# Performance work log

Hardware: AMD Instinct MI355X
Metric: run time of the kernel (lower is better)

## Reference

```python
import jax, jax.numpy as jnp
import numpy as np

N = 50000      # nodes
E = 600000     # edges
G = 512        # graphs in batch
F_IN = 128     # input node features
H = 128        # hidden size (both layers)
PH = 128       # pool/classifier hidden size


def setup_inputs() -> dict:
    key = jax.random.key(0)
    ks = jax.random.split(key, 12)
    def lin(k, fi, fo):
        return (jax.random.normal(k, (fi, fo), jnp.float32) / np.sqrt(fi)).astype(jnp.float32)
    return {
        "x": jax.random.normal(ks[0], (N, F_IN), jnp.float32),
        "edge_index": jax.random.randint(ks[1], (2, E), 0, N),
        "batch": jnp.sort(jax.random.randint(ks[2], (N,), 0, G)),
        "W1": lin(ks[3], F_IN, H), "b1": jnp.zeros((H,), jnp.float32),
        "ln1_g": jnp.ones((H,), jnp.float32), "ln1_b": jnp.zeros((H,), jnp.float32),
        "W2": lin(ks[4], H, H), "b2": jnp.zeros((H,), jnp.float32),
        "ln2_g": jnp.ones((H,), jnp.float32), "ln2_b": jnp.zeros((H,), jnp.float32),
        "gate_w1": lin(ks[5], H, PH), "gate_b1": jnp.zeros((PH,), jnp.float32),
        "gate_w2": lin(ks[6], PH, 1), "gate_b2": jnp.zeros((1,), jnp.float32),
        "cls_w1": lin(ks[7], H, PH), "cls_b1": jnp.zeros((PH,), jnp.float32),
        "cls_w2": lin(ks[8], PH, 2), "cls_b2": jnp.zeros((2,), jnp.float32),
    }


def _layer_norm(h, g, b):
    m = h.mean(-1, keepdims=True)
    v = ((h - m) ** 2).mean(-1, keepdims=True)
    return (h - m) * jax.lax.rsqrt(v + 1e-5) * g + b


def _gcn(x, src, dst, norm, W, b):
    # GCNConv: x' = D^{-1/2} (A+I) D^{-1/2} (x W) + b
    h = x @ W
    out = jax.ops.segment_sum(h[src] * norm[:, None], dst, num_segments=N)
    return out + b


def reference(x, edge_index, batch, W1, b1, ln1_g, ln1_b, W2, b2, ln2_g, ln2_b,
              gate_w1, gate_b1, gate_w2, gate_b2, cls_w1, cls_b1, cls_w2, cls_b2):
    loops = jnp.arange(N, dtype=edge_index.dtype)
    src = jnp.concatenate([edge_index[0], loops])
    dst = jnp.concatenate([edge_index[1], loops])
    deg = jax.ops.segment_sum(jnp.ones_like(src, dtype=x.dtype), dst, num_segments=N)
    dinv = jnp.where(deg > 0, jax.lax.rsqrt(jnp.maximum(deg, 1e-12)), 0.0)
    norm = dinv[src] * dinv[dst]  # [(E+N)]

    h = jax.nn.relu(_layer_norm(_gcn(x, src, dst, norm, W1, b1), ln1_g, ln1_b))
    h = jax.nn.relu(_layer_norm(_gcn(h, src, dst, norm, W2, b2), ln2_g, ln2_b))

    # GlobalAttention pooling: gate MLP -> scatter softmax over graphs -> weighted sum
    gate = (jax.nn.relu(h @ gate_w1 + gate_b1) @ gate_w2 + gate_b2)[:, 0]  # [N]
    gmax = jax.ops.segment_max(gate, batch, num_segments=G)
    a = jnp.exp(gate - gmax[batch])
    denom = jax.ops.segment_sum(a, batch, num_segments=G)
    alpha = a / denom[batch]
    pooled = jax.ops.segment_sum(alpha[:, None] * h, batch, num_segments=G)  # [G, H]

    logits = jax.nn.relu(pooled @ cls_w1 + cls_b1) @ cls_w2 + cls_b2  # [G, 2]
    return logits
```

## Files before the change

kernel.cpp:

```cpp
#include <hip/hip_runtime.h>
#include <hip/hip_bf16.h>

typedef short s8v __attribute__((ext_vector_type(8)));
typedef float f4v __attribute__((ext_vector_type(4)));

__device__ __forceinline__ unsigned short f2bf(float f) {
  unsigned int u = __builtin_bit_cast(unsigned int, f);
  unsigned int r = u + 0x7fffu + ((u >> 16) & 1u);
  return (unsigned short)(r >> 16);
}
__device__ __forceinline__ float bf2f(unsigned short s) {
  return __builtin_bit_cast(float, ((unsigned int)s) << 16);
}
__device__ __forceinline__ float bflo(unsigned int v) {
  return __builtin_bit_cast(float, (unsigned int)(v << 16));
}
__device__ __forceinline__ float bfhi(unsigned int v) {
  return __builtin_bit_cast(float, (unsigned int)(v & 0xffff0000u));
}
__device__ __forceinline__ unsigned int packbf(float a, float b) {
  return (unsigned int)f2bf(a) | ((unsigned int)f2bf(b) << 16);
}

__device__ __forceinline__ int lower_bound_i(const int* a, int n, int key) {
  int lo = 0, hi = n;
  while (lo < hi) { int mid = (lo + hi) >> 1; if (a[mid] < key) lo = mid + 1; else hi = mid; }
  return lo;
}

__global__ __launch_bounds__(256) void pack_zero(
    const float* __restrict__ Wa, const float* __restrict__ Wb, const float* __restrict__ Wc,
    unsigned short* __restrict__ P, unsigned int* __restrict__ deg, int n) {
  int bid = blockIdx.x;
  if (bid >= 384) {
    int i = (bid - 384) * 256 + threadIdx.x;
    if (i < n) deg[i] = 0u;
    return;
  }
  int gidx = bid * 256 + threadIdx.x;
  int which = gidx >> 15;
  int idx = gidx & 32767;
  const float* W = (which == 0) ? Wa : (which == 1) ? Wb : Wc;
  int j = idx & 15;
  int lane = (idx >> 4) & 63;
  int t = (idx >> 10) & 7;
  int c = (idx >> 13) & 3;
  int k = c * 32 + (lane >> 4) * 8 + (j & 7);
  int nn = t * 16 + (lane & 15);
  float f = W[k * 128 + nn];
  unsigned short hi = f2bf(f);
  unsigned short outv = (j < 8) ? hi : f2bf(f - bf2f(hi));
  P[gidx] = outv;
}

__global__ void accum_deg(const int* __restrict__ dst, unsigned int* __restrict__ deg, int E) {
  int e = blockIdx.x * blockDim.x + threadIdx.x;
  if (e < E) atomicAdd(&deg[dst[e]], 1u);
}

__global__ __launch_bounds__(256) void scanA(const unsigned int* __restrict__ deg,
                                             int* __restrict__ offs, int* __restrict__ partial,
                                             float* __restrict__ dinv, int n) {
  __shared__ int sh[256];
  int t = threadIdx.x;
  int i = blockIdx.x * 256 + t;
  int v = (i < n) ? (int)deg[i] : 0;
  if (i < n) dinv[i] = rsqrtf((float)(deg[i] + 1u));
  sh[t] = v;
  __syncthreads();
  for (int o = 1; o < 256; o <<= 1) {
    int add = (t >= o) ? sh[t - o] : 0;
    __syncthreads();
    sh[t] += add;
    __syncthreads();
  }
  if (i < n) offs[i] = sh[t] - v;
  if (t == 255) partial[blockIdx.x] = sh[255];
}

__global__ __launch_bounds__(256) void scanC(int* __restrict__ offs, const int* __restrict__ partial,
                                             int* __restrict__ cursor, int n, int E) {
  __shared__ int red[256];
  int bid = blockIdx.x;
  int t = threadIdx.x;
  int s = 0;
  for (int j = t; j < bid; j += 256) s += partial[j];
  red[t] = s;
  __syncthreads();
#pragma unroll
  for (int o = 128; o > 0; o >>= 1) {
    if (t < o) red[t] += red[t + o];
    __syncthreads();
  }
  int pre = red[0];
  int i = bid * 256 + t;
  if (i < n) {
    int o = offs[i] + pre;
    offs[i] = o;
    cursor[i] = o;
  }
  if (i == 0) offs[n] = E;
}

__global__ __launch_bounds__(256) void gemm1_scatter(
    const float* __restrict__ in, const unsigned short* __restrict__ P,
    unsigned short* __restrict__ out, int n,
    const int* __restrict__ src, const int* __restrict__ dst,
    int* __restrict__ cursor, int2* __restrict__ col2,
    const float* __restrict__ dinv, int E, int gemmBlocks) {
  if ((int)blockIdx.x >= gemmBlocks) {
    int e = ((int)blockIdx.x - gemmBlocks) * 256 + threadIdx.x;
    if (e < E) {
      int d = dst[e];
      int s = src[e];
      int slot = atomicAdd(&cursor[d], 1);
      col2[slot] = make_int2(s, __builtin_bit_cast(int, dinv[s]));
    }
    return;
  }
  int tid = threadIdx.x;
  int wave = tid >> 6, lane = tid & 63;
  int quad = lane >> 4, col = lane & 15;
  int base = blockIdx.x * 64 + wave * 16;
  int m = base + col;

  f4v acc[8];
#pragma unroll
  for (int t = 0; t < 8; ++t) acc[t] = (f4v){0.f, 0.f, 0.f, 0.f};

  for (int c = 0; c < 4; ++c) {
    s8v ah, al;
    float v[8];
    if (m < n) {
      const float4* xp = reinterpret_cast<const float4*>(in + (size_t)m * 128 + c * 32 + quad * 8);
      float4 v0 = xp[0], v1 = xp[1];
      v[0] = v0.x; v[1] = v0.y; v[2] = v0.z; v[3] = v0.w;
      v[4] = v1.x; v[5] = v1.y; v[6] = v1.z; v[7] = v1.w;
    } else {
#pragma unroll
      for (int j = 0; j < 8; ++j) v[j] = 0.f;
    }
#pragma unroll
    for (int j = 0; j < 8; ++j) {
      unsigned short h = f2bf(v[j]);
      ah[j] = (short)h;
      al[j] = (short)f2bf(v[j] - bf2f(h));
    }
#pragma unroll
    for (int t = 0; t < 8; ++t) {
      const s8v* bp = reinterpret_cast<const s8v*>(&P[((c * 8 + t) * 64 + lane) * 16]);
      s8v bh = bp[0], bl = bp[1];
      acc[t] = __builtin_amdgcn_mfma_f32_16x16x32_bf16(ah, bh, acc[t], 0, 0, 0);
      acc[t] = __builtin_amdgcn_mfma_f32_16x16x32_bf16(ah, bl, acc[t], 0, 0, 0);
      acc[t] = __builtin_amdgcn_mfma_f32_16x16x32_bf16(al, bh, acc[t], 0, 0, 0);
    }
  }
#pragma unroll
  for (int t = 0; t < 8; ++t)
#pragma unroll
    for (int r = 0; r < 4; ++r) {
      int mm = base + quad * 4 + r;
      if (mm < n) out[(size_t)mm * 128 + t * 16 + col] = f2bf(acc[t][r]);
    }
}

__global__ __launch_bounds__(256) void gemm_b16in(
    const unsigned short* __restrict__ in, const unsigned short* __restrict__ P,
    unsigned short* __restrict__ out, int n) {
  int tid = threadIdx.x;
  int wave = tid >> 6, lane = tid & 63;
  int quad = lane >> 4, col = lane & 15;
  int base = blockIdx.x * 64 + wave * 16;
  int m = base + col;

  f4v acc[8];
#pragma unroll
  for (int t = 0; t < 8; ++t) acc[t] = (f4v){0.f, 0.f, 0.f, 0.f};

  for (int c = 0; c < 4; ++c) {
    s8v ah;
    if (m < n)
      ah = *reinterpret_cast<const s8v*>(in + (size_t)m * 128 + c * 32 + quad * 8);
    else
      ah = (s8v){0, 0, 0, 0, 0, 0, 0, 0};
#pragma unroll
    for (int t = 0; t < 8; ++t) {
      const s8v* bp = reinterpret_cast<const s8v*>(&P[((c * 8 + t) * 64 + lane) * 16]);
      s8v bh = bp[0], bl = bp[1];
      acc[t] = __builtin_amdgcn_mfma_f32_16x16x32_bf16(ah, bh, acc[t], 0, 0, 0);
      acc[t] = __builtin_amdgcn_mfma_f32_16x16x32_bf16(ah, bl, acc[t], 0, 0, 0);
    }
  }
#pragma unroll
  for (int t = 0; t < 8; ++t)
#pragma unroll
    for (int r = 0; r < 4; ++r) {
      int mm = base + quad * 4 + r;
      if (mm < n) out[(size_t)mm * 128 + t * 16 + col] = f2bf(acc[t][r]);
    }
}

__global__ __launch_bounds__(256) void gemm_gate(
    const unsigned short* __restrict__ in, const unsigned short* __restrict__ P,
    const float* __restrict__ gb1, const float* __restrict__ gw2,
    const float* __restrict__ gb2, float* __restrict__ gate, int n) {
  int tid = threadIdx.x;
  int wave = tid >> 6, lane = tid & 63;
  int quad = lane >> 4, col = lane & 15;
  int base = blockIdx.x * 64 + wave * 16;
  int m = base + col;

  f4v acc[8];
#pragma unroll
  for (int t = 0; t < 8; ++t) acc[t] = (f4v){0.f, 0.f, 0.f, 0.f};

  for (int c = 0; c < 4; ++c) {
    s8v ah;
    if (m < n)
      ah = *reinterpret_cast<const s8v*>(in + (size_t)m * 128 + c * 32 + quad * 8);
    else
      ah = (s8v){0, 0, 0, 0, 0, 0, 0, 0};
#pragma unroll
    for (int t = 0; t < 8; ++t) {
      const s8v* bp = reinterpret_cast<const s8v*>(&P[((c * 8 + t) * 64 + lane) * 16]);
      s8v bh = bp[0], bl = bp[1];
      acc[t] = __builtin_amdgcn_mfma_f32_16x16x32_bf16(ah, bh, acc[t], 0, 0, 0);
      acc[t] = __builtin_amdgcn_mfma_f32_16x16x32_bf16(ah, bl, acc[t], 0, 0, 0);
    }
  }
  float bv[8], g2[8];
#pragma unroll
  for (int t = 0; t < 8; ++t) {
    bv[t] = gb1[t * 16 + col];
    g2[t] = gw2[t * 16 + col];
  }
  float gb2v = gb2[0];
#pragma unroll
  for (int r = 0; r < 4; ++r) {
    float p = 0.f;
#pragma unroll
    for (int t = 0; t < 8; ++t)
      p += fmaxf(acc[t][r] + bv[t], 0.f) * g2[t];
#pragma unroll
    for (int o = 1; o < 16; o <<= 1) p += __shfl_xor(p, o);
    int mm = base + quad * 4 + r;
    if (col == 0 && mm < n) gate[mm] = p + gb2v;
  }
}

__global__ __launch_bounds__(256) void gather_ln(
    const int* __restrict__ offs, const int2* __restrict__ col2,
    const float* __restrict__ dinv, const unsigned short* __restrict__ h,
    const float* __restrict__ bias, const float* __restrict__ gam,
    const float* __restrict__ bet, unsigned short* __restrict__ out, int n) {
  int wid = (int)((blockIdx.x * 256u + threadIdx.x) >> 6);
  int lane = threadIdx.x & 63;
  int grp = lane >> 4;
  int sub = lane & 15;
  int i = wid * 4 + grp;
  if (i >= n) return;
  const uint4* hu = reinterpret_cast<const uint4*>(h);
  float di = dinv[i];
  float sl = di * di;
  uint4 hv = hu[(size_t)i * 16 + sub];
  float4 b0v = reinterpret_cast<const float4*>(bias)[sub * 2];
  float4 b1v = reinterpret_cast<const float4*>(bias)[sub * 2 + 1];
  float v[8];
  v[0] = bflo(hv.x) * sl + b0v.x; v[1] = bfhi(hv.x) * sl + b0v.y;
  v[2] = bflo(hv.y) * sl + b0v.z; v[3] = bfhi(hv.y) * sl + b0v.w;
  v[4] = bflo(hv.z) * sl + b1v.x; v[5] = bfhi(hv.z) * sl + b1v.y;
  v[6] = bflo(hv.w) * sl + b1v.z; v[7] = bfhi(hv.w) * sl + b1v.w;
  int b0 = offs[i], b1 = offs[i + 1];
  int e = b0;
  for (; e + 4 <= b1; e += 4) {
    int2 c0 = col2[e], c1 = col2[e + 1], c2 = col2[e + 2], c3 = col2[e + 3];
    uint4 h0 = hu[(size_t)c0.x * 16 + sub];
    uint4 h1 = hu[(size_t)c1.x * 16 + sub];
    uint4 h2 = hu[(size_t)c2.x * 16 + sub];
    uint4 h3 = hu[(size_t)c3.x * 16 + sub];
    float n0 = __builtin_bit_cast(float, c0.y) * di;
    float n1 = __builtin_bit_cast(float, c1.y) * di;
    float n2 = __builtin_bit_cast(float, c2.y) * di;
    float n3 = __builtin_bit_cast(float, c3.y) * di;
    v[0] += bflo(h0.x) * n0 + bflo(h1.x) * n1 + bflo(h2.x) * n2 + bflo(h3.x) * n3;
    v[1] += bfhi(h0.x) * n0 + bfhi(h1.x) * n1 + bfhi(h2.x) * n2 + bfhi(h3.x) * n3;
    v[2] += bflo(h0.y) * n0 + bflo(h1.y) * n1 + bflo(h2.y) * n2 + bflo(h3.y) * n3;
    v[3] += bfhi(h0.y) * n0 + bfhi(h1.y) * n1 + bfhi(h2.y) * n2 + bfhi(h3.y) * n3;
    v[4] += bflo(h0.z) * n0 + bflo(h1.z) * n1 + bflo(h2.z) * n2 + bflo(h3.z) * n3;
    v[5] += bfhi(h0.z) * n0 + bfhi(h1.z) * n1 + bfhi(h2.z) * n2 + bfhi(h3.z) * n3;
    v[6] += bflo(h0.w) * n0 + bflo(h1.w) * n1 + bflo(h2.w) * n2 + bflo(h3.w) * n3;
    v[7] += bfhi(h0.w) * n0 + bfhi(h1.w) * n1 + bfhi(h2.w) * n2 + bfhi(h3.w) * n3;
  }
  for (; e < b1; ++e) {
    int2 c0 = col2[e];
    uint4 h0 = hu[(size_t)c0.x * 16 + sub];
    float n0 = __builtin_bit_cast(float, c0.y) * di;
    v[0] += bflo(h0.x) * n0; v[1] += bfhi(h0.x) * n0;
    v[2] += bflo(h0.y) * n0; v[3] += bfhi(h0.y) * n0;
    v[4] += bflo(h0.z) * n0; v[5] += bfhi(h0.z) * n0;
    v[6] += bflo(h0.w) * n0; v[7] += bfhi(h0.w) * n0;
  }
  float s = 0.f, q = 0.f;
#pragma unroll
  for (int j = 0; j < 8; ++j) { s += v[j]; q += v[j] * v[j]; }
#pragma unroll
  for (int o = 1; o < 16; o <<= 1) {
    s += __shfl_xor(s, o);
    q += __shfl_xor(q, o);
  }
  float m = s * (1.0f / 128.0f);
  float var = q * (1.0f / 128.0f) - m * m;
  float rs = rsqrtf(var + 1e-5f);
  float4 g0 = reinterpret_cast<const float4*>(gam)[sub * 2];
  float4 g1 = reinterpret_cast<const float4*>(gam)[sub * 2 + 1];
  float4 e0 = reinterpret_cast<const float4*>(bet)[sub * 2];
  float4 e1 = reinterpret_cast<const float4*>(bet)[sub * 2 + 1];
  uint4 ov;
  ov.x = packbf(fmaxf((v[0] - m) * rs * g0.x + e0.x, 0.f), fmaxf((v[1] - m) * rs * g0.y + e0.y, 0.f));
  ov.y = packbf(fmaxf((v[2] - m) * rs * g0.z + e0.z, 0.f), fmaxf((v[3] - m) * rs * g0.w + e0.w, 0.f));
  ov.z = packbf(fmaxf((v[4] - m) * rs * g1.x + e1.x, 0.f), fmaxf((v[5] - m) * rs * g1.y + e1.y, 0.f));
  ov.w = packbf(fmaxf((v[6] - m) * rs * g1.z + e1.z, 0.f), fmaxf((v[7] - m) * rs * g1.w + e1.w, 0.f));
  reinterpret_cast<uint4*>(out)[(size_t)i * 16 + sub] = ov;
}

__global__ __launch_bounds__(256) void pool_cls(
    float* __restrict__ gate, const unsigned short* __restrict__ h,
    const int* __restrict__ batch,
    const float* __restrict__ w1, const float* __restrict__ b1,
    const float* __restrict__ w2, const float* __restrict__ b2,
    float* __restrict__ out, int n) {
  int g = blockIdx.x;
  int tid = threadIdx.x;
  __shared__ float red[256];
  __shared__ float red2[256];
  __shared__ float p[128];
  __shared__ float r[128];
  int lo = lower_bound_i(batch, n, g);
  int hi = lower_bound_i(batch, n, g + 1);
  if (lo >= hi) {
    if (tid < 128) p[tid] = 0.0f;
  } else {
    float m = -3.0e38f;
    for (int i = lo + tid; i < hi; i += 256) m = fmaxf(m, gate[i]);
    red[tid] = m;
    __syncthreads();
#pragma unroll
    for (int o = 128; o > 0; o >>= 1) {
      if (tid < o) red[tid] = fmaxf(red[tid], red[tid + o]);
      __syncthreads();
    }
    m = red[0];
    __syncthreads();
    float s = 0.0f;
    for (int i = lo + tid; i < hi; i += 256) {
      float e = __expf(gate[i] - m);
      gate[i] = e;
      s += e;
    }
    red[tid] = s;
    __syncthreads();
#pragma unroll
    for (int o = 128; o > 0; o >>= 1) {
      if (tid < o) red[tid] += red[tid + o];
      __syncthreads();
    }
    float inv = 1.0f / red[0];
    __syncthreads();
    const unsigned int* hu = reinterpret_cast<const unsigned int*>(h);
    int j = tid & 63, rgp = tid >> 6;
    float a0 = 0.f, a1 = 0.f;
    int i = lo + rgp;
    for (; i + 4 < hi; i += 8) {
      unsigned int p0 = hu[(size_t)i * 64 + j];
      unsigned int p1 = hu[(size_t)(i + 4) * 64 + j];
      float w0 = gate[i], w1v = gate[i + 4];
      a0 += bflo(p0) * w0 + bflo(p1) * w1v;
      a1 += bfhi(p0) * w0 + bfhi(p1) * w1v;
    }
    if (i < hi) {
      unsigned int p0 = hu[(size_t)i * 64 + j];
      float w0 = gate[i];
      a0 += bflo(p0) * w0;
      a1 += bfhi(p0) * w0;
    }
    red[tid] = a0;
    red2[tid] = a1;
    __syncthreads();
    if (tid < 64) {
      p[2 * tid]     = (red[tid] + red[tid + 64] + red[tid + 128] + red[tid + 192]) * inv;
      p[2 * tid + 1] = (red2[tid] + red2[tid + 64] + red2[tid + 128] + red2[tid + 192]) * inv;
    }
  }
  __syncthreads();
  int j = tid & 127, half = tid >> 7;
  float acc = 0.0f;
#pragma unroll 8
  for (int k = half * 64; k < half * 64 + 64; ++k)
    acc = fmaf(p[k], w1[k * 128 + j], acc);
  red[tid] = acc;
  __syncthreads();
  if (tid < 128) r[tid] = fmaxf(red[tid] + red[tid + 128] + b1[tid], 0.0f);
  __syncthreads();
  if (tid < 2) {
    float a = 0.0f;
    for (int k = 0; k < 128; ++k) a = fmaf(r[k], w2[k * 2 + tid], a);
    out[g * 2 + tid] = a + b2[tid];
  }
}

static inline size_t alup(size_t x) { return (x + 255) & ~(size_t)255; }

extern "C" void kernel_launch(void* const* d_in, const int* in_sizes, int n_in,
                              void* d_out, int out_size, void* d_ws, size_t ws_size,
                              hipStream_t stream) {
  const float* x    = (const float*)d_in[0];
  const int*   ei   = (const int*)d_in[1];
  const int*   bat  = (const int*)d_in[2];
  const float* W1   = (const float*)d_in[3];
  const float* b1   = (const float*)d_in[4];
  const float* ln1g = (const float*)d_in[5];
  const float* ln1b = (const float*)d_in[6];
  const float* W2   = (const float*)d_in[7];
  const float* b2   = (const float*)d_in[8];
  const float* ln2g = (const float*)d_in[9];
  const float* ln2b = (const float*)d_in[10];
  const float* gw1  = (const float*)d_in[11];
  const float* gb1  = (const float*)d_in[12];
  const float* gw2  = (const float*)d_in[13];
  const float* gb2  = (const float*)d_in[14];
  const float* cw1  = (const float*)d_in[15];
  const float* cb1  = (const float*)d_in[16];
  const float* cw2  = (const float*)d_in[17];
  const float* cb2  = (const float*)d_in[18];

  const int N = in_sizes[2];
  const int E = in_sizes[1] / 2;
  const int G = out_size / 2;
  const int* src = ei;
  const int* dst = ei + E;

  int nb256 = (N + 255) / 256;
  int eb256 = (E + 255) / 256;
  int mfmaB = (N + 63) / 64;
  int gatherB = (N + 15) / 16;

  char* base = (char*)d_ws;
  unsigned int* deg = (unsigned int*)base; base += alup((size_t)N * 4);
  float* dinv = (float*)base;              base += alup((size_t)N * 4);
  int* offs = (int*)base;                  base += alup((size_t)(N + 1) * 4);
  int* cursor = (int*)base;                base += alup((size_t)N * 4);
  int* partial = (int*)base;               base += alup((size_t)nb256 * 4);
  int2* col2 = (int2*)base;                base += alup((size_t)E * 8);
  unsigned short* pW = (unsigned short*)base; base += alup((size_t)3 * 32768 * 2);
  unsigned short* hbuf = (unsigned short*)base; base += alup((size_t)N * 128 * 2);
  unsigned short* hout = (unsigned short*)base; base += alup((size_t)N * 128 * 2);
  float* gate = (float*)base;              base += alup((size_t)N * 4);

  unsigned short* pW1 = pW;
  unsigned short* pW2 = pW + 32768;
  unsigned short* pG1 = pW + 65536;

  float* out = (float*)d_out;

  pack_zero<<<384 + nb256, 256, 0, stream>>>(W1, W2, gw1, pW, deg, N);
  accum_deg<<<eb256, 256, 0, stream>>>(dst, deg, E);
  scanA<<<nb256, 256, 0, stream>>>(deg, offs, partial, dinv, N);
  scanC<<<nb256, 256, 0, stream>>>(offs, partial, cursor, N, E);
  gemm1_scatter<<<mfmaB + eb256, 256, 0, stream>>>(x, pW1, hbuf, N,
                                                   src, dst, cursor, col2, dinv, E, mfmaB);
  gather_ln<<<gatherB, 256, 0, stream>>>(offs, col2, dinv, hbuf, b1, ln1g, ln1b, hout, N);
  gemm_b16in<<<mfmaB, 256, 0, stream>>>(hout, pW2, hbuf, N);
  gather_ln<<<gatherB, 256, 0, stream>>>(offs, col2, dinv, hbuf, b2, ln2g, ln2b, hout, N);
  gemm_gate<<<mfmaB, 256, 0, stream>>>(hout, pG1, gb1, gw2, gb2, gate, N);
  pool_cls<<<G, 256, 0, stream>>>(gate, hout, bat, cw1, cb1, cw2, cb2, out, N);
}
```

Baseline: 272.5 us.

## Fuse neighbor gather + LayerNorm into following GEMM via shared-memory tile

Each gather+LayerNorm+ReLU pass now writes its 64-node output tile into LDS, and the same block immediately runs the MFMA GEMM for the next layer (W2 or the gate MLP) on that tile. Two kernel launches and a full N x 128 bf16 round trip through global memory per layer are removed. The second fused kernel still writes h to global for pooling. The cost is coarser blocks (64 nodes per block), a block barrier between the irregular gather phase and the GEMM phase, and extra LDS use that may lower occupancy while the latency-bound gather runs.

```diff
diff --git a/kernel.cpp b/kernel.cpp
--- a/kernel.cpp
+++ b/kernel.cpp
@@ -3,6 +3,8 @@
 
 typedef short s8v __attribute__((ext_vector_type(8)));
 typedef float f4v __attribute__((ext_vector_type(4)));
+
+#define LDA 136
 
 __device__ __forceinline__ unsigned short f2bf(float f) {
   unsigned int u = __builtin_bit_cast(unsigned int, f);
@@ -28,244 +30,15 @@
   return lo;
 }
 
-__global__ __launch_bounds__(256) void pack_zero(
-    const float* __restrict__ Wa, const float* __restrict__ Wb, const float* __restrict__ Wc,
-    unsigned short* __restrict__ P, unsigned int* __restrict__ deg, int n) {
-  int bid = blockIdx.x;
-  if (bid >= 384) {
-    int i = (bid - 384) * 256 + threadIdx.x;
-    if (i < n) deg[i] = 0u;
-    return;
-  }
-  int gidx = bid * 256 + threadIdx.x;
-  int which = gidx >> 15;
-  int idx = gidx & 32767;
-  const float* W = (which == 0) ? Wa : (which == 1) ? Wb : Wc;
-  int j = idx & 15;
-  int lane = (idx >> 4) & 63;
-  int t = (idx >> 10) & 7;
-  int c = (idx >> 13) & 3;
-  int k = c * 32 + (lane >> 4) * 8 + (j & 7);
-  int nn = t * 16 + (lane & 15);
-  float f = W[k * 128 + nn];
-  unsigned short hi = f2bf(f);
-  unsigned short outv = (j < 8) ? hi : f2bf(f - bf2f(hi));
-  P[gidx] = outv;
-}
-
-__global__ void accum_deg(const int* __restrict__ dst, unsigned int* __restrict__ deg, int E) {
-  int e = blockIdx.x * blockDim.x + threadIdx.x;
-  if (e < E) atomicAdd(&deg[dst[e]], 1u);
-}
-
-__global__ __launch_bounds__(256) void scanA(const unsigned int* __restrict__ deg,
-                                             int* __restrict__ offs, int* __restrict__ partial,
-                                             float* __restrict__ dinv, int n) {
-  __shared__ int sh[256];
-  int t = threadIdx.x;
-  int i = blockIdx.x * 256 + t;
-  int v = (i < n) ? (int)deg[i] : 0;
-  if (i < n) dinv[i] = rsqrtf((float)(deg[i] + 1u));
-  sh[t] = v;
-  __syncthreads();
-  for (int o = 1; o < 256; o <<= 1) {
-    int add = (t >= o) ? sh[t - o] : 0;
-    __syncthreads();
-    sh[t] += add;
-    __syncthreads();
-  }
-  if (i < n) offs[i] = sh[t] - v;
-  if (t == 255) partial[blockIdx.x] = sh[255];
-}
-
-__global__ __launch_bounds__(256) void scanC(int* __restrict__ offs, const int* __restrict__ partial,
-                                             int* __restrict__ cursor, int n, int E) {
-  __shared__ int red[256];
-  int bid = blockIdx.x;
-  int t = threadIdx.x;
-  int s = 0;
-  for (int j = t; j < bid; j += 256) s += partial[j];
-  red[t] = s;
-  __syncthreads();
-#pragma unroll
-  for (int o = 128; o > 0; o >>= 1) {
-    if (t < o) red[t] += red[t + o];
-    __syncthreads();
-  }
-  int pre = red[0];
-  int i = bid * 256 + t;
-  if (i < n) {
-    int o = offs[i] + pre;
-    offs[i] = o;
-    cursor[i] = o;
-  }
-  if (i == 0) offs[n] = E;
-}
-
-__global__ __launch_bounds__(256) void gemm1_scatter(
-    const float* __restrict__ in, const unsigned short* __restrict__ P,
-    unsigned short* __restrict__ out, int n,
-    const int* __restrict__ src, const int* __restrict__ dst,
-    int* __restrict__ cursor, int2* __restrict__ col2,
-    const float* __restrict__ dinv, int E, int gemmBlocks) {
-  if ((int)blockIdx.x >= gemmBlocks) {
-    int e = ((int)blockIdx.x - gemmBlocks) * 256 + threadIdx.x;
-    if (e < E) {
-      int d = dst[e];
-      int s = src[e];
-      int slot = atomicAdd(&cursor[d], 1);
-      col2[slot] = make_int2(s, __builtin_bit_cast(int, dinv[s]));
-    }
-    return;
-  }
-  int tid = threadIdx.x;
-  int wave = tid >> 6, lane = tid & 63;
-  int quad = lane >> 4, col = lane & 15;
-  int base = blockIdx.x * 64 + wave * 16;
-  int m = base + col;
-
-  f4v acc[8];
-#pragma unroll
-  for (int t = 0; t < 8; ++t) acc[t] = (f4v){0.f, 0.f, 0.f, 0.f};
-
-  for (int c = 0; c < 4; ++c) {
-    s8v ah, al;
-    float v[8];
-    if (m < n) {
-      const float4* xp = reinterpret_cast<const float4*>(in + (size_t)m * 128 + c * 32 + quad * 8);
-      float4 v0 = xp[0], v1 = xp[1];
-      v[0] = v0.x; v[1] = v0.y; v[2] = v0.z; v[3] = v0.w;
-      v[4] = v1.x; v[5] = v1.y; v[6] = v1.z; v[7] = v1.w;
-    } else {
-#pragma unroll
-      for (int j = 0; j < 8; ++j) v[j] = 0.f;
-    }
-#pragma unroll
-    for (int j = 0; j < 8; ++j) {
-      unsigned short h = f2bf(v[j]);
-      ah[j] = (short)h;
-      al[j] = (short)f2bf(v[j] - bf2f(h));
-    }
-#pragma unroll
-    for (int t = 0; t < 8; ++t) {
-      const s8v* bp = reinterpret_cast<const s8v*>(&P[((c * 8 + t) * 64 + lane) * 16]);
-      s8v bh = bp[0], bl = bp[1];
-      acc[t] = __builtin_amdgcn_mfma_f32_16x16x32_bf16(ah, bh, acc[t], 0, 0, 0);
-      acc[t] = __builtin_amdgcn_mfma_f32_16x16x32_bf16(ah, bl, acc[t], 0, 0, 0);
-      acc[t] = __builtin_amdgcn_mfma_f32_16x16x32_bf16(al, bh, acc[t], 0, 0, 0);
-    }
-  }
-#pragma unroll
-  for (int t = 0; t < 8; ++t)
-#pragma unroll
-    for (int r = 0; r < 4; ++r) {
-      int mm = base + quad * 4 + r;
-      if (mm < n) out[(size_t)mm * 128 + t * 16 + col] = f2bf(acc[t][r]);
-    }
-}
-
-__global__ __launch_bounds__(256) void gemm_b16in(
-    const unsigned short* __restrict__ in, const unsigned short* __restrict__ P,
-    unsigned short* __restrict__ out, int n) {
-  int tid = threadIdx.x;
-  int wave = tid >> 6, lane = tid & 63;
-  int quad = lane >> 4, col = lane & 15;
-  int base = blockIdx.x * 64 + wave * 16;
-  int m = base + col;
-
-  f4v acc[8];
-#pragma unroll
-  for (int t = 0; t < 8; ++t) acc[t] = (f4v){0.f, 0.f, 0.f, 0.f};
-
-  for (int c = 0; c < 4; ++c) {
-    s8v ah;
-    if (m < n)
-      ah = *reinterpret_cast<const s8v*>(in + (size_t)m * 128 + c * 32 + quad * 8);
-    else
-      ah = (s8v){0, 0, 0, 0, 0, 0, 0, 0};
-#pragma unroll
-    for (int t = 0; t < 8; ++t) {
-      const s8v* bp = reinterpret_cast<const s8v*>(&P[((c * 8 + t) * 64 + lane) * 16]);
-      s8v bh = bp[0], bl = bp[1];
-      acc[t] = __builtin_amdgcn_mfma_f32_16x16x32_bf16(ah, bh, acc[t], 0, 0, 0);
-      acc[t] = __builtin_amdgcn_mfma_f32_16x16x32_bf16(ah, bl, acc[t], 0, 0, 0);
-    }
-  }
-#pragma unroll
-  for (int t = 0; t < 8; ++t)
-#pragma unroll
-    for (int r = 0; r < 4; ++r) {
-      int mm = base + quad * 4 + r;
-      if (mm < n) out[(size_t)mm * 128 + t * 16 + col] = f2bf(acc[t][r]);
-    }
-}
-
-__global__ __launch_bounds__(256) void gemm_gate(
-    const unsigned short* __restrict__ in, const unsigned short* __restrict__ P,
-    const float* __restrict__ gb1, const float* __restrict__ gw2,
-    const float* __restrict__ gb2, float* __restrict__ gate, int n) {
-  int tid = threadIdx.x;
-  int wave = tid >> 6, lane = tid & 63;
-  int quad = lane >> 4, col = lane & 15;
-  int base = blockIdx.x * 64 + wave * 16;
-  int m = base + col;
-
-  f4v acc[8];
-#pragma unroll
-  for (int t = 0; t < 8; ++t) acc[t] = (f4v){0.f, 0.f, 0.f, 0.f};
-
-  for (int c = 0; c < 4; ++c) {
-    s8v ah;
-    if (m < n)
-      ah = *reinterpret_cast<const s8v*>(in + (size_t)m * 128 + c * 32 + quad * 8);
-    else
-      ah = (s8v){0, 0, 0, 0, 0, 0, 0, 0};
-#pragma unroll
-    for (int t = 0; t < 8; ++t) {
-      const s8v* bp = reinterpret_cast<const s8v*>(&P[((c * 8 + t) * 64 + lane) * 16]);
-      s8v bh = bp[0], bl = bp[1];
-      acc[t] = __builtin_amdgcn_mfma_f32_16x16x32_bf16(ah, bh, acc[t], 0, 0, 0);
-      acc[t] = __builtin_amdgcn_mfma_f32_16x16x32_bf16(ah, bl, acc[t], 0, 0, 0);
-    }
-  }
-  float bv[8], g2[8];
-#pragma unroll
-  for (int t = 0; t < 8; ++t) {
-    bv[t] = gb1[t * 16 + col];
-    g2[t] = gw2[t * 16 + col];
-  }
-  float gb2v = gb2[0];
-#pragma unroll
-  for (int r = 0; r < 4; ++r) {
-    float p = 0.f;
-#pragma unroll
-    for (int t = 0; t < 8; ++t)
-      p += fmaxf(acc[t][r] + bv[t], 0.f) * g2[t];
-#pragma unroll
-    for (int o = 1; o < 16; o <<= 1) p += __shfl_xor(p, o);
-    int mm = base + quad * 4 + r;
-    if (col == 0 && mm < n) gate[mm] = p + gb2v;
-  }
-}
-
-__global__ __launch_bounds__(256) void gather_ln(
-    const int* __restrict__ offs, const int2* __restrict__ col2,
-    const float* __restrict__ dinv, const unsigned short* __restrict__ h,
-    const float* __restrict__ bias, const float* __restrict__ gam,
-    const float* __restrict__ bet, unsigned short* __restrict__ out, int n) {
-  int wid = (int)((blockIdx.x * 256u + threadIdx.x) >> 6);
-  int lane = threadIdx.x & 63;
-  int grp = lane >> 4;
-  int sub = lane & 15;
-  int i = wid * 4 + grp;
-  if (i >= n) return;
-  const uint4* hu = reinterpret_cast<const uint4*>(h);
+__device__ __forceinline__ void gather_node(
+    int i, int sub, const int* __restrict__ offs, const int2* __restrict__ col2,
+    const float* __restrict__ dinv, const uint4* __restrict__ hu,
+    const float* __restrict__ bias, float v[8]) {
   float di = dinv[i];
   float sl = di * di;
   uint4 hv = hu[(size_t)i * 16 + sub];
   float4 b0v = reinterpret_cast<const float4*>(bias)[sub * 2];
   float4 b1v = reinterpret_cast<const float4*>(bias)[sub * 2 + 1];
-  float v[8];
   v[0] = bflo(hv.x) * sl + b0v.x; v[1] = bfhi(hv.x) * sl + b0v.y;
   v[2] = bflo(hv.y) * sl + b0v.z; v[3] = bfhi(hv.y) * sl + b0v.w;
   v[4] = bflo(hv.z) * sl + b1v.x; v[5] = bfhi(hv.z) * sl + b1v.y;
@@ -300,6 +73,10 @@
     v[4] += bflo(h0.z) * n0; v[5] += bfhi(h0.z) * n0;
     v[6] += bflo(h0.w) * n0; v[7] += bfhi(h0.w) * n0;
   }
+}
+
+__device__ __forceinline__ uint4 ln_relu_pack(
+    float v[8], int sub, const float* __restrict__ gam, const float* __restrict__ bet) {
   float s = 0.f, q = 0.f;
 #pragma unroll
   for (int j = 0; j < 8; ++j) { s += v[j]; q += v[j] * v[j]; }
@@ -320,7 +97,257 @@
   ov.y = packbf(fmaxf((v[2] - m) * rs * g0.z + e0.z, 0.f), fmaxf((v[3] - m) * rs * g0.w + e0.w, 0.f));
   ov.z = packbf(fmaxf((v[4] - m) * rs * g1.x + e1.x, 0.f), fmaxf((v[5] - m) * rs * g1.y + e1.y, 0.f));
   ov.w = packbf(fmaxf((v[6] - m) * rs * g1.z + e1.z, 0.f), fmaxf((v[7] - m) * rs * g1.w + e1.w, 0.f));
-  reinterpret_cast<uint4*>(out)[(size_t)i * 16 + sub] = ov;
+  return ov;
+}
+
+__global__ __launch_bounds__(256) void pack_zero(
+    const float* __restrict__ Wa, const float* __restrict__ Wb, const float* __restrict__ Wc,
+    unsigned short* __restrict__ P, unsigned int* __restrict__ deg, int n) {
+  int bid = blockIdx.x;
+  if (bid >= 384) {
+    int i = (bid - 384) * 256 + threadIdx.x;
+    if (i < n) deg[i] = 0u;
+    return;
+  }
+  int gidx = bid * 256 + threadIdx.x;
+  int which = gidx >> 15;
+  int idx = gidx & 32767;
+  const float* W = (which == 0) ? Wa : (which == 1) ? Wb : Wc;
+  int j = idx & 15;
+  int lane = (idx >> 4) & 63;
+  int t = (idx >> 10) & 7;
+  int c = (idx >> 13) & 3;
+  int k = c * 32 + (lane >> 4) * 8 + (j & 7);
+  int nn = t * 16 + (lane & 15);
+  float f = W[k * 128 + nn];
+  unsigned short hi = f2bf(f);
+  unsigned short outv = (j < 8) ? hi : f2bf(f - bf2f(hi));
+  P[gidx] = outv;
+}
+
+__global__ void accum_deg(const int* __restrict__ dst, unsigned int* __restrict__ deg, int E) {
+  int e = blockIdx.x * blockDim.x + threadIdx.x;
+  if (e < E) atomicAdd(&deg[dst[e]], 1u);
+}
+
+__global__ __launch_bounds__(256) void scanA(const unsigned int* __restrict__ deg,
+                                             int* __restrict__ offs, int* __restrict__ partial,
+                                             float* __restrict__ dinv, int n) {
+  __shared__ int sh[256];
+  int t = threadIdx.x;
+  int i = blockIdx.x * 256 + t;
+  int v = (i < n) ? (int)deg[i] : 0;
+  if (i < n) dinv[i] = rsqrtf((float)(deg[i] + 1u));
+  sh[t] = v;
+  __syncthreads();
+  for (int o = 1; o < 256; o <<= 1) {
+    int add = (t >= o) ? sh[t - o] : 0;
+    __syncthreads();
+    sh[t] += add;
+    __syncthreads();
+  }
+  if (i < n) offs[i] = sh[t] - v;
+  if (t == 255) partial[blockIdx.x] = sh[255];
+}
+
+__global__ __launch_bounds__(256) void scanC(int* __restrict__ offs, const int* __restrict__ partial,
+                                             int* __restrict__ cursor, int n, int E) {
+  __shared__ int red[256];
+  int bid = blockIdx.x;
+  int t = threadIdx.x;
+  int s = 0;
+  for (int j = t; j < bid; j += 256) s += partial[j];
+  red[t] = s;
+  __syncthreads();
+#pragma unroll
+  for (int o = 128; o > 0; o >>= 1) {
+    if (t < o) red[t] += red[t + o];
+    __syncthreads();
+  }
+  int pre = red[0];
+  int i = bid * 256 + t;
+  if (i < n) {
+    int o = offs[i] + pre;
+    offs[i] = o;
+    cursor[i] = o;
+  }
+  if (i == 0) offs[n] = E;
+}
+
+__global__ __launch_bounds__(256) void gemm1_scatter(
+    const float* __restrict__ in, const unsigned short* __restrict__ P,
+    unsigned short* __restrict__ out, int n,
+    const int* __restrict__ src, const int* __restrict__ dst,
+    int* __restrict__ cursor, int2* __restrict__ col2,
+    const float* __restrict__ dinv, int E, int gemmBlocks) {
+  if ((int)blockIdx.x >= gemmBlocks) {
+    int e = ((int)blockIdx.x - gemmBlocks) * 256 + threadIdx.x;
+    if (e < E) {
+      int d = dst[e];
+      int s = src[e];
+      int slot = atomicAdd(&cursor[d], 1);
+      col2[slot] = make_int2(s, __builtin_bit_cast(int, dinv[s]));
+    }
+    return;
+  }
+  int tid = threadIdx.x;
+  int wave = tid >> 6, lane = tid & 63;
+  int quad = lane >> 4, col = lane & 15;
+  int base = blockIdx.x * 64 + wave * 16;
+  int m = base + col;
+
+  f4v acc[8];
+#pragma unroll
+  for (int t = 0; t < 8; ++t) acc[t] = (f4v){0.f, 0.f, 0.f, 0.f};
+
+  for (int c = 0; c < 4; ++c) {
+    s8v ah, al;
+    float v[8];
+    if (m < n) {
+      const float4* xp = reinterpret_cast<const float4*>(in + (size_t)m * 128 + c * 32 + quad * 8);
+      float4 v0 = xp[0], v1 = xp[1];
+      v[0] = v0.x; v[1] = v0.y; v[2] = v0.z; v[3] = v0.w;
+      v[4] = v1.x; v[5] = v1.y; v[6] = v1.z; v[7] = v1.w;
+    } else {
+#pragma unroll
+      for (int j = 0; j < 8; ++j) v[j] = 0.f;
+    }
+#pragma unroll
+    for (int j = 0; j < 8; ++j) {
+      unsigned short h = f2bf(v[j]);
+      ah[j] = (short)h;
+      al[j] = (short)f2bf(v[j] - bf2f(h));
+    }
+#pragma unroll
+    for (int t = 0; t < 8; ++t) {
+      const s8v* bp = reinterpret_cast<const s8v*>(&P[((c * 8 + t) * 64 + lane) * 16]);
+      s8v bh = bp[0], bl = bp[1];
+      acc[t] = __builtin_amdgcn_mfma_f32_16x16x32_bf16(ah, bh, acc[t], 0, 0, 0);
+      acc[t] = __builtin_amdgcn_mfma_f32_16x16x32_bf16(ah, bl, acc[t], 0, 0, 0);
+      acc[t] = __builtin_amdgcn_mfma_f32_16x16x32_bf16(al, bh, acc[t], 0, 0, 0);
+    }
+  }
+#pragma unroll
+  for (int t = 0; t < 8; ++t)
+#pragma unroll
+    for (int r = 0; r < 4; ++r) {
+      int mm = base + quad * 4 + r;
+      if (mm < n) out[(size_t)mm * 128 + t * 16 + col] = f2bf(acc[t][r]);
+    }
+}
+
+__global__ __launch_bounds__(256) void gather_gemm(
+    const int* __restrict__ offs, const int2* __restrict__ col2,
+    const float* __restrict__ dinv, const unsigned short* __restrict__ h,
+    const float* __restrict__ bias, const float* __restrict__ gam,
+    const float* __restrict__ bet, const unsigned short* __restrict__ P,
+    unsigned short* __restrict__ out, int n) {
+  __shared__ unsigned short A[64 * LDA];
+  int tid = threadIdx.x;
+  int wave = tid >> 6, lane = tid & 63;
+  int grp = lane >> 4, sub = lane & 15;
+  const uint4* hu = reinterpret_cast<const uint4*>(h);
+  int blk = blockIdx.x * 64;
+  for (int it = 0; it < 4; ++it) {
+    int li = it * 16 + wave * 4 + grp;
+    int i = blk + li;
+    uint4 ov;
+    if (i < n) {
+      float v[8];
+      gather_node(i, sub, offs, col2, dinv, hu, bias, v);
+      ov = ln_relu_pack(v, sub, gam, bet);
+    } else {
+      ov = make_uint4(0u, 0u, 0u, 0u);
+    }
+    *reinterpret_cast<uint4*>(&A[li * LDA + sub * 8]) = ov;
+  }
+  __syncthreads();
+  int quad = lane >> 4, col = lane & 15;
+  f4v acc[8];
+#pragma unroll
+  for (int t = 0; t < 8; ++t) acc[t] = (f4v){0.f, 0.f, 0.f, 0.f};
+  int liA = wave * 16 + col;
+  for (int c = 0; c < 4; ++c) {
+    s8v ah = *reinterpret_cast<const s8v*>(&A[liA * LDA + c * 32 + quad * 8]);
+#pragma unroll
+    for (int t = 0; t < 8; ++t) {
+      const s8v* bp = reinterpret_cast<const s8v*>(&P[((c * 8 + t) * 64 + lane) * 16]);
+      s8v bh = bp[0], bl = bp[1];
+      acc[t] = __builtin_amdgcn_mfma_f32_16x16x32_bf16(ah, bh, acc[t], 0, 0, 0);
+      acc[t] = __builtin_amdgcn_mfma_f32_16x16x32_bf16(ah, bl, acc[t], 0, 0, 0);
+    }
+  }
+#pragma unroll
+  for (int t = 0; t < 8; ++t)
+#pragma unroll
+    for (int r = 0; r < 4; ++r) {
+      int mm = blk + wave * 16 + quad * 4 + r;
+      if (mm < n) out[(size_t)mm * 128 + t * 16 + col] = f2bf(acc[t][r]);
+    }
+}
+
+__global__ __launch_bounds__(256) void gather_gate(
+    const int* __restrict__ offs, const int2* __restrict__ col2,
+    const float* __restrict__ dinv, const unsigned short* __restrict__ h,
+    const float* __restrict__ bias, const float* __restrict__ gam,
+    const float* __restrict__ bet, const unsigned short* __restrict__ P,
+    const float* __restrict__ gb1, const float* __restrict__ gw2,
+    const float* __restrict__ gb2, unsigned short* __restrict__ hout,
+    float* __restrict__ gate, int n) {
+  __shared__ unsigned short A[64 * LDA];
+  int tid = threadIdx.x;
+  int wave = tid >> 6, lane = tid & 63;
+  int grp = lane >> 4, sub = lane & 15;
+  const uint4* hu = reinterpret_cast<const uint4*>(h);
+  int blk = blockIdx.x * 64;
+  for (int it = 0; it < 4; ++it) {
+    int li = it * 16 + wave * 4 + grp;
+    int i = blk + li;
+    uint4 ov;
+    if (i < n) {
+      float v[8];
+      gather_node(i, sub, offs, col2, dinv, hu, bias, v);
+      ov = ln_relu_pack(v, sub, gam, bet);
+      reinterpret_cast<uint4*>(hout)[(size_t)i * 16 + sub] = ov;
+    } else {
+      ov = make_uint4(0u, 0u, 0u, 0u);
+    }
+    *reinterpret_cast<uint4*>(&A[li * LDA + sub * 8]) = ov;
+  }
+  __syncthreads();
+  int quad = lane >> 4, col = lane & 15;
+  f4v acc[8];
+#pragma unroll
+  for (int t = 0; t < 8; ++t) acc[t] = (f4v){0.f, 0.f, 0.f, 0.f};
+  int liA = wave * 16 + col;
+  for (int c = 0; c < 4; ++c) {
+    s8v ah = *reinterpret_cast<const s8v*>(&A[liA * LDA + c * 32 + quad * 8]);
+#pragma unroll
+    for (int t = 0; t < 8; ++t) {
+      const s8v* bp = reinterpret_cast<const s8v*>(&P[((c * 8 + t) * 64 + lane) * 16]);
+      s8v bh = bp[0], bl = bp[1];
+      acc[t] = __builtin_amdgcn_mfma_f32_16x16x32_bf16(ah, bh, acc[t], 0, 0, 0);
+      acc[t] = __builtin_amdgcn_mfma_f32_16x16x32_bf16(ah, bl, acc[t], 0, 0, 0);
+    }
+  }
+  float bv[8], g2[8];
+#pragma unroll
+  for (int t = 0; t < 8; ++t) {
+    bv[t] = gb1[t * 16 + col];
+    g2[t] = gw2[t * 16 + col];
+  }
+  float gb2v = gb2[0];
+#pragma unroll
+  for (int r = 0; r < 4; ++r) {
+    float p = 0.f;
+#pragma unroll
+    for (int t = 0; t < 8; ++t)
+      p += fmaxf(acc[t][r] + bv[t], 0.f) * g2[t];
+#pragma unroll
+    for (int o = 1; o < 16; o <<= 1) p += __shfl_xor(p, o);
+    int mm = blk + wave * 16 + quad * 4 + r;
+    if (col == 0 && mm < n) gate[mm] = p + gb2v;
+  }
 }
 
 __global__ __launch_bounds__(256) void pool_cls(
@@ -442,7 +469,6 @@
   int nb256 = (N + 255) / 256;
   int eb256 = (E + 255) / 256;
   int mfmaB = (N + 63) / 64;
-  int gatherB = (N + 15) / 16;
 
   char* base = (char*)d_ws;
   unsigned int* deg = (unsigned int*)base; base += alup((size_t)N * 4);
@@ -452,8 +478,9 @@
   int* partial = (int*)base;               base += alup((size_t)nb256 * 4);
   int2* col2 = (int2*)base;                base += alup((size_t)E * 8);
   unsigned short* pW = (unsigned short*)base; base += alup((size_t)3 * 32768 * 2);
-  unsigned short* hbuf = (unsigned short*)base; base += alup((size_t)N * 128 * 2);
-  unsigned short* hout = (unsigned short*)base; base += alup((size_t)N * 128 * 2);
+  unsigned short* hbuf = (unsigned short*)base;  base += alup((size_t)N * 128 * 2);
+  unsigned short* hbuf2 = (unsigned short*)base; base += alup((size_t)N * 128 * 2);
+  unsigned short* hout = (unsigned short*)base;  base += alup((size_t)N * 128 * 2);
   float* gate = (float*)base;              base += alup((size_t)N * 4);
 
   unsigned short* pW1 = pW;
@@ -468,9 +495,9 @@
   scanC<<<nb256, 256, 0, stream>>>(offs, partial, cursor, N, E);
   gemm1_scatter<<<mfmaB + eb256, 256, 0, stream>>>(x, pW1, hbuf, N,
                                                    src, dst, cursor, col2, dinv, E, mfmaB);
-  gather_ln<<<gatherB, 256, 0, stream>>>(offs, col2, dinv, hbuf, b1, ln1g, ln1b, hout, N);
-  gemm_b16in<<<mfmaB, 256, 0, stream>>>(hout, pW2, hbuf, N);
-  gather_ln<<<gatherB, 256, 0, stream>>>(offs, col2, dinv, hbuf, b2, ln2g, ln2b, hout, N);
-  gemm_gate<<<mfmaB, 256, 0, stream>>>(hout, pG1, gb1, gw2, gb2, gate, N);
+  gather_gemm<<<mfmaB, 256, 0, stream>>>(offs, col2, dinv, hbuf, b1, ln1g, ln1b,
+                                         pW2, hbuf2, N);
+  gather_gate<<<mfmaB, 256, 0, stream>>>(offs, col2, dinv, hbuf2, b2, ln2g, ln2b,
+                                         pG1, gb1, gw2, gb2, hout, gate, N);
   pool_cls<<<G, 256, 0, stream>>>(gate, hout, bat, cw1, cb1, cw2, cb2, out, N);
 }
```

Result: faster. 266.0 us (-2.4%).
